# Optimization experiments

Hardware: AMD Instinct MI355X
Metric: run time of the kernel (lower is better)

## Reference

```python
import jax, jax.numpy as jnp
import numpy as np

B, CIN, H, W = 8, 256, 128, 128
DIM, K, NCLS = 32, 2048, 20
M, T = 0.999, 0.4
N_SEL = B * H * W // 2  # sal masks have exactly half foreground


def _l2norm(x, axis):
    n = jnp.sqrt(jnp.sum(x * x, axis=axis, keepdims=True))
    return x / jnp.maximum(n, 1e-12)


def _balanced_bce(logits, labels):
    # BalancedCrossEntropyLoss (astmt-style), size_average=True
    labels = (labels >= 0.5).astype(logits.dtype)
    n_pos = jnp.sum(labels)
    n_neg = labels.size - n_pos
    gz = (logits >= 0).astype(logits.dtype)
    # stable log-sigmoid formulation
    loss_val = logits * (labels - gz) - jnp.log1p(jnp.exp(logits - 2.0 * logits * gz))
    loss_pos = jnp.sum(-labels * loss_val)
    loss_neg = jnp.sum(-(1.0 - labels) * loss_val)
    tot = n_pos + n_neg
    return (n_neg / tot * loss_pos + n_pos / tot * loss_neg) / labels.size


def setup_inputs() -> dict:
    key = jax.random.key(0)
    ks = jax.random.split(key, 8)
    im_q = jax.random.normal(ks[0], (B, CIN, H, W), dtype=jnp.float32)
    im_k = jax.random.normal(ks[1], (B, CIN, H, W), dtype=jnp.float32)
    # checkerboard saliency: exactly half the pixels are foreground
    sal = (jnp.arange(B * H * W, dtype=jnp.int32) % 2).reshape(B, H, W)
    W_q = jax.random.normal(ks[2], (DIM, CIN), dtype=jnp.float32) * 0.05
    W_bg = jax.random.normal(ks[3], (1, CIN), dtype=jnp.float32) * 0.05
    W_k = jax.random.normal(ks[4], (DIM, CIN), dtype=jnp.float32) * 0.05
    W_cls = jax.random.normal(ks[5], (NCLS, DIM), dtype=jnp.float32) * 0.05
    q0 = jax.random.normal(ks[6], (DIM, K), dtype=jnp.float32)
    obj_queue = _l2norm(q0, 0)
    return {"im_q": im_q, "sal_q": sal, "im_k": im_k, "sal_k": sal,
            "W_q": W_q, "W_bg": W_bg, "W_k": W_k, "W_cls": W_cls,
            "obj_queue": obj_queue}


def reference(im_q, sal_q, im_k, sal_k, W_q, W_bg, W_k, W_cls, obj_queue):
    # --- query encoder (1x1-conv feature head + bg head) ---
    q = jnp.einsum('oc,bchw->bohw', W_q, im_q)          # [B, DIM, H, W]
    q = _l2norm(q, 1)
    q_bg = jnp.einsum('oc,bchw->bohw', W_bg, im_q)[:, 0]  # [B, H, W]
    sal_loss = _balanced_bce(q_bg, sal_q.astype(q.dtype))

    # --- classifier (1x1 conv) ---
    cluster = jnp.einsum('oc,bchw->bhwo', W_cls, q).reshape(-1, NCLS)

    # --- pixel -> image-index labeling via saliency mask ---
    offset = jnp.arange(0, 2 * B, 2, dtype=sal_q.dtype)
    lab = ((sal_q + offset[:, None, None]) * sal_q).reshape(-1)
    mask_indexes = jnp.nonzero(lab, size=N_SEL, fill_value=0)[0]
    sal_sel = lab[mask_indexes] // 2                     # [N_SEL] image index per fg pixel

    # --- momentum key encoder + object prototypes (no grad) ---
    W_k_m = M * W_k + (1.0 - M) * W_q
    k = jnp.einsum('oc,bchw->bohw', W_k_m, im_k)
    k = _l2norm(k, 1).reshape(B, DIM, H * W)
    salk = sal_k.reshape(B, H * W).astype(k.dtype)
    protos = _l2norm(jnp.einsum('bdn,bn->bd', k, salk), 1)  # [B, DIM]

    # --- gather foreground pixels ---
    q_flat = q.transpose(0, 2, 3, 1).reshape(-1, DIM)
    q_sel = q_flat[mask_indexes]                          # [N_SEL, DIM]
    cl_sel = cluster[mask_indexes]
    # opt == 2: keep only per-pixel max cluster logit, pseudo labels are zeros
    cl_sel = jnp.max(cl_sel, axis=1, keepdims=True)       # [N_SEL, 1]
    pseudo_labels = jnp.zeros((N_SEL,), dtype=jnp.int32)

    # --- contrastive logits: drop own prototype column per row ---
    batch_logits = q_sel @ protos.T                       # [N_SEL, B]
    cols = jnp.arange(B - 1)
    take = cols[None, :] + (cols[None, :] >= sal_sel[:, None]).astype(cols.dtype)
    batch_logits = jnp.take_along_axis(batch_logits, take, axis=1)  # [N_SEL, B-1]

    bank_logits = q_sel @ obj_queue                       # [N_SEL, K]
    logits = jnp.concatenate([cl_sel, batch_logits, bank_logits], axis=1) / T

    # --- dequeue-and-enqueue (ptr = 0) ---
    new_queue = jax.lax.dynamic_update_slice(obj_queue, protos.T, (0, 0))
    return logits, pseudo_labels, sal_loss, new_queue
```

## Files before the change

kernel.cpp:

```cpp
#include <hip/hip_runtime.h>

typedef __attribute__((ext_vector_type(8))) short short8;
typedef __attribute__((ext_vector_type(4))) float f32x4;
typedef __attribute__((ext_vector_type(2))) float f32x2;

constexpr int CIN  = 256;
constexpr int HWp  = 16384;
constexpr int NSEL = 65536;
constexpr int NCOLS = 2056;

constexpr size_t OUT_PL   = (size_t)NSEL * NCOLS;
constexpr size_t OUT_LOSS = OUT_PL + NSEL;
constexpr size_t OUT_NQ   = OUT_LOSS + 1;

constexpr size_t WS_TILECNT  = 0;
constexpr size_t WS_TILEBASE = 2048;
constexpr size_t WS_NPOS     = 4096;
constexpr size_t WS_LPLN     = 4104;
constexpr size_t WS_WQT      = 8192;
constexpr size_t WS_WKMT     = 40960;
constexpr size_t WS_PSUM     = 73728;
constexpr size_t WS_PROTO    = 74752;
constexpr size_t WS_QT       = 131072;
constexpr size_t WS_CLSEL    = 262144;
constexpr size_t WS_SALSEL   = 524288;
constexpr size_t WS_QSEL     = 1048576;

static __device__ __forceinline__ unsigned short f2bf(float f) {
  const unsigned x = __float_as_uint(f);
  return (unsigned short)((x + 0x7fffu + ((x >> 16) & 1u)) >> 16);
}
static __device__ __forceinline__ float bf2f(unsigned short u) {
  return __uint_as_float(((unsigned)u) << 16);
}

__global__ __launch_bounds__(256) void kP1(const int* __restrict__ salq, int* __restrict__ tileCnt,
                                           const float* __restrict__ Wq, const float* __restrict__ Wk,
                                           float* __restrict__ wqt, float* __restrict__ wkmt,
                                           float* __restrict__ psum, float* __restrict__ lpln) {
  const int g = blockIdx.x, t = threadIdx.x;
  __shared__ int red[256];
  const int base = g << 9;
  red[t] = ((salq[base + 2 * t] != 0) ? 1 : 0) + ((salq[base + 2 * t + 1] != 0) ? 1 : 0);
  __syncthreads();
  for (int s = 128; s > 0; s >>= 1) { if (t < s) red[t] += red[t + s]; __syncthreads(); }
  if (t == 0) tileCnt[g] = red[0];
  if (g < 32) {
    const int idx = (g << 8) + t;
    const int o = idx & 31, c = idx >> 5;
    const float wq = Wq[o * 256 + c];
    wqt[idx] = wq;
    wkmt[idx] = 0.999f * Wk[o * 256 + c] + 0.001f * wq;
  }
  if (g == 32) { psum[t] = 0.f; if (t < 2) lpln[t] = 0.f; }
}

__global__ __launch_bounds__(256) void kP2(const int* __restrict__ tileCnt, int* __restrict__ tileBase,
                                           int* __restrict__ nposp) {
  const int t = threadIdx.x;
  __shared__ int sc[256];
  const int c0 = tileCnt[t];
  sc[t] = c0;
  __syncthreads();
  for (int off = 1; off < 256; off <<= 1) {
    int v = (t >= off) ? sc[t - off] : 0;
    __syncthreads();
    sc[t] += v;
    __syncthreads();
  }
  tileBase[t] = sc[t] - c0;
  if (t == 255) *nposp = sc[255];
}

__global__ __launch_bounds__(256) void kAB(
    const float* __restrict__ imq, const float* __restrict__ imk,
    const int* __restrict__ salq, const int* __restrict__ salk,
    const float* __restrict__ wqt, const float* __restrict__ wkmt,
    const float* __restrict__ wbg, const float* __restrict__ wcls,
    const int* __restrict__ tileBase,
    ushort* __restrict__ qsel, float* __restrict__ clsel, int* __restrict__ salsel,
    float* __restrict__ lpln, float* __restrict__ psum) {
  const int g = ((blockIdx.x & 7) << 6) + (blockIdx.x >> 3);
  const int t = threadIdx.x;
  const bool isA = (g < 256);
  const int tile = isA ? g : (g - 256);
  const int base = tile << 9;
  const int b = base >> 14;
  const int n = (base & (HWp - 1)) + (t << 1);
  const float* __restrict__ ip = (isA ? imq : imk) + (size_t)b * (CIN * HWp) + n;
  const float* __restrict__ wt0 = isA ? wqt : wkmt;

  float a0[32], a1[32];
#pragma unroll
  for (int o = 0; o < 32; ++o) { a0[o] = 0.f; a1[o] = 0.f; }
  float bg0 = 0.f, bg1 = 0.f;

#pragma unroll 8
  for (int c = 0; c < 256; ++c) {
    const f32x2 v = __builtin_nontemporal_load(
        reinterpret_cast<const f32x2*>(ip + (size_t)c * HWp));
    const float* wt = wt0 + (c << 5);
    const float wb = wbg[c];
#pragma unroll
    for (int o = 0; o < 32; ++o) {
      a0[o] = fmaf(wt[o], v.x, a0[o]);
      a1[o] = fmaf(wt[o], v.y, a1[o]);
    }
    bg0 = fmaf(wb, v.x, bg0);
    bg1 = fmaf(wb, v.y, bg1);
  }

  const int lane = t & 63, wv = t >> 6;
  const int flat0 = base + (t << 1);

  if (isA) {
    const int s0 = (salq[flat0] != 0) ? 1 : 0;
    const int s1 = (salq[flat0 + 1] != 0) ? 1 : 0;
    const unsigned spair = (unsigned)(s0 + s1);
    unsigned incl = spair;
#pragma unroll
    for (int off = 1; off < 64; off <<= 1) {
      unsigned u = __shfl_up(incl, off);
      if (lane >= off) incl += u;
    }
    __shared__ int wtot[4];
    if (lane == 63) wtot[wv] = (int)incl;
    __syncthreads();
    int wbase = 0;
    for (int i = 0; i < wv; ++i) wbase += wtot[i];
    const int excl = tileBase[tile] + wbase + (int)(incl - spair);

#pragma unroll
    for (int i = 0; i < 2; ++i) {
      const int si = i ? s1 : s0;
      const int rank = i ? (excl + s0) : excl;
      if (si && rank < NSEL) {
        float ss = 0.f;
#pragma unroll
        for (int o = 0; o < 32; ++o) { const float a = i ? a1[o] : a0[o]; ss = fmaf(a, a, ss); }
        const float inv = 1.f / fmaxf(sqrtf(ss), 1e-12f);
        float qn[32];
#pragma unroll
        for (int o = 0; o < 32; ++o) qn[o] = (i ? a1[o] : a0[o]) * inv;
        float m = -3.402823466e38f;
#pragma unroll
        for (int j = 0; j < 20; ++j) {
          float d = 0.f;
#pragma unroll
          for (int o = 0; o < 32; ++o) d = fmaf(wcls[(j << 5) + o], qn[o], d);
          m = fmaxf(m, d);
        }
        clsel[rank] = m;
        salsel[rank] = b;
        ushort* qp = qsel + ((size_t)rank << 5);
#pragma unroll
        for (int v4 = 0; v4 < 4; ++v4) {
          short8 v8;
#pragma unroll
          for (int j = 0; j < 8; ++j) v8[j] = (short)f2bf(qn[(v4 << 3) + j]);
          *reinterpret_cast<short8*>(qp + (v4 << 3)) = v8;
        }
      }
    }
    const float gz0 = (bg0 >= 0.f) ? 1.f : 0.f;
    const float gz1 = (bg1 >= 0.f) ? 1.f : 0.f;
    const float lv0 = bg0 * ((float)s0 - gz0) - log1pf(expf(bg0 - 2.f * bg0 * gz0));
    const float lv1 = bg1 * ((float)s1 - gz1) - log1pf(expf(bg1 - 2.f * bg1 * gz1));
    float lp = -(s0 ? lv0 : 0.f) - (s1 ? lv1 : 0.f);
    float ln = -(s0 ? 0.f : lv0) - (s1 ? 0.f : lv1);
#pragma unroll
    for (int off = 32; off > 0; off >>= 1) { lp += __shfl_down(lp, off); ln += __shfl_down(ln, off); }
    __shared__ float slp[4], sln[4];
    if (lane == 0) { slp[wv] = lp; sln[wv] = ln; }
    __syncthreads();
    if (t == 0) {
      atomicAdd(&lpln[0], slp[0] + slp[1] + slp[2] + slp[3]);
      atomicAdd(&lpln[1], sln[0] + sln[1] + sln[2] + sln[3]);
    }
  } else {
    const int s0 = (salk[flat0] != 0) ? 1 : 0;
    const int s1 = (salk[flat0 + 1] != 0) ? 1 : 0;
    float ss0 = 0.f, ss1 = 0.f;
#pragma unroll
    for (int o = 0; o < 32; ++o) { ss0 = fmaf(a0[o], a0[o], ss0); ss1 = fmaf(a1[o], a1[o], ss1); }
    const float inv0 = s0 ? (1.f / fmaxf(sqrtf(ss0), 1e-12f)) : 0.f;
    const float inv1 = s1 ? (1.f / fmaxf(sqrtf(ss1), 1e-12f)) : 0.f;
    float p[32];
#pragma unroll
    for (int o = 0; o < 32; ++o) p[o] = a0[o] * inv0 + a1[o] * inv1;
#pragma unroll
    for (int o = 0; o < 32; ++o) {
#pragma unroll
      for (int off = 32; off > 0; off >>= 1) p[o] += __shfl_down(p[o], off);
    }
    __shared__ float sp[4][32];
    if (lane == 0) {
#pragma unroll
      for (int o = 0; o < 32; ++o) sp[wv][o] = p[o];
    }
    __syncthreads();
    if (t < 32) atomicAdd(&psum[(b << 5) + t], sp[0][t] + sp[1][t] + sp[2][t] + sp[3][t]);
  }
}

__global__ __launch_bounds__(256) void kC(const float* __restrict__ objq, const float* __restrict__ psum,
                                          const float* __restrict__ lpln, const int* __restrict__ nposp,
                                          float* __restrict__ proto, ushort* __restrict__ qt,
                                          float* __restrict__ nq, float* __restrict__ outLoss) {
  const int g = blockIdx.x, t = threadIdx.x;
  if (g == 256) {
    __shared__ float sq[256];
    __shared__ float sinv[8];
    const float v = psum[t];
    sq[t] = v * v;
    __syncthreads();
    if (t < 8) {
      float s = 0.f;
      for (int o = 0; o < 32; ++o) s += sq[(t << 5) + o];
      sinv[t] = 1.f / fmaxf(sqrtf(s), 1e-12f);
    }
    __syncthreads();
    const float pv = v * sinv[t >> 5];
    proto[t] = pv;
    const int p = t >> 5, o = t & 31;
    nq[(size_t)o * 2048 + p] = pv;
    if (t == 0) {
      const float np = (float)(*nposp);
      outLoss[0] = ((131072.f - np) / 131072.f * lpln[0] + np / 131072.f * lpln[1]) / 131072.f;
    }
  } else {
    const int idx = (g << 8) + t;
    const int o = idx >> 11, j = idx & 2047;
    const float v = objq[idx];
    qt[(j << 5) + o] = f2bf(v);
    if (j >= 8) nq[idx] = v;
  }
}

__global__ __launch_bounds__(256) void kDE(const ushort* __restrict__ qsel, const ushort* __restrict__ qt,
                                           const float* __restrict__ proto, const float* __restrict__ clsel,
                                           const int* __restrict__ salsel,
                                           float* __restrict__ out, int* __restrict__ pl) {
  __shared__ float buf[16][524];
  __shared__ float dd[16][9];
  const int t = threadIdx.x;
  const int g = ((blockIdx.x & 7) << 9) + (blockIdx.x >> 3);
  const int wv = t >> 6, lane = t & 63;
  const int r0 = g << 4;
  if (t < 16) pl[r0 + t] = 0;

  const int rlo = lane & 15, kh = lane >> 4;
  const f32x4 zero = {0.f, 0.f, 0.f, 0.f};

  const short8 bfrag = *reinterpret_cast<const short8*>(
      qsel + (size_t)(r0 + rlo) * 32 + kh * 8);
  const ushort* qa = qt + rlo * 32 + kh * 8;
  float* obase = out + (size_t)r0 * NCOLS;

  if (t < 128) {
    const int ri = t >> 3, pp = t & 7;
    const short8* qp = reinterpret_cast<const short8*>(qsel + ((size_t)(r0 + ri) << 5));
    float s = 0.f;
#pragma unroll
    for (int i = 0; i < 4; ++i) {
      const short8 v8 = qp[i];
#pragma unroll
      for (int j = 0; j < 8; ++j)
        s = fmaf(proto[(pp << 5) + (i << 3) + j], bf2f((unsigned short)v8[j]), s);
    }
    dd[ri][pp] = s;
  }
  __syncthreads();

  if (t < 16) {
    const int b = salsel[r0 + t];
    buf[t][0] = clsel[r0 + t] * 2.5f;
#pragma unroll
    for (int c = 0; c < 7; ++c) {
      const int pi = c + ((c >= b) ? 1 : 0);
      buf[t][1 + c] = dd[t][pi] * 2.5f;
    }
  }
#pragma unroll
  for (int ct2 = 0; ct2 < 8; ++ct2) {
    const int lt = (wv << 3) + ct2;
    const short8 afrag = *reinterpret_cast<const short8*>(qa + (size_t)lt * 512);
    f32x4 r = __builtin_amdgcn_mfma_f32_16x16x32_bf16(afrag, bfrag, zero, 0, 0, 0);
    r *= 2.5f;
    *reinterpret_cast<f32x4*>(&buf[rlo][8 + (lt << 4) + (kh << 2)]) = r;
  }
  __syncthreads();
#pragma unroll
  for (int i = 0; i < 9; ++i) {
    const int w4 = (i << 8) + t;
    if (w4 < 2080) {
      const int row = w4 / 130;
      const int c4 = w4 - row * 130;
      const f32x4 v = *reinterpret_cast<const f32x4*>(&buf[row][c4 << 2]);
      __builtin_nontemporal_store(v, reinterpret_cast<f32x4*>(obase + (size_t)row * NCOLS + (c4 << 2)));
    }
  }
  __syncthreads();

  for (int p = 1; p < 4; ++p) {
#pragma unroll
    for (int ct2 = 0; ct2 < 8; ++ct2) {
      const int lt = (wv << 3) + ct2;
      const short8 afrag = *reinterpret_cast<const short8*>(qa + (size_t)((p << 5) + lt) * 512);
      f32x4 r = __builtin_amdgcn_mfma_f32_16x16x32_bf16(afrag, bfrag, zero, 0, 0, 0);
      r *= 2.5f;
      *reinterpret_cast<f32x4*>(&buf[rlo][(lt << 4) + (kh << 2)]) = r;
    }
    __syncthreads();
    const int cbase = 8 + (p << 9);
#pragma unroll
    for (int i = 0; i < 8; ++i) {
      const int w4 = (i << 8) + t;
      const int row = w4 >> 7;
      const int c4 = w4 & 127;
      const f32x4 v = *reinterpret_cast<const f32x4*>(&buf[row][c4 << 2]);
      __builtin_nontemporal_store(v, reinterpret_cast<f32x4*>(obase + (size_t)row * NCOLS + cbase + (c4 << 2)));
    }
    __syncthreads();
  }
}

extern "C" void kernel_launch(void* const* d_in, const int* in_sizes, int n_in,
                              void* d_out, int out_size, void* d_ws, size_t ws_size,
                              hipStream_t stream) {
  const float* imq  = (const float*)d_in[0];
  const int*   salq = (const int*)d_in[1];
  const float* imk  = (const float*)d_in[2];
  const int*   salk = (const int*)d_in[3];
  const float* Wq   = (const float*)d_in[4];
  const float* Wbg  = (const float*)d_in[5];
  const float* Wk   = (const float*)d_in[6];
  const float* Wcls = (const float*)d_in[7];
  const float* objq = (const float*)d_in[8];
  float* out = (float*)d_out;
  char* ws = (char*)d_ws;

  int*    tileCnt  = (int*)(ws + WS_TILECNT);
  int*    tileBase = (int*)(ws + WS_TILEBASE);
  int*    nposp    = (int*)(ws + WS_NPOS);
  float*  lpln     = (float*)(ws + WS_LPLN);
  float*  wqt      = (float*)(ws + WS_WQT);
  float*  wkmt     = (float*)(ws + WS_WKMT);
  float*  psum     = (float*)(ws + WS_PSUM);
  float*  proto    = (float*)(ws + WS_PROTO);
  ushort* qt       = (ushort*)(ws + WS_QT);
  float*  clsel    = (float*)(ws + WS_CLSEL);
  int*    salsel   = (int*)(ws + WS_SALSEL);
  ushort* qsel     = (ushort*)(ws + WS_QSEL);

  hipLaunchKernelGGL(kP1, dim3(256), dim3(256), 0, stream, salq, tileCnt, Wq, Wk, wqt, wkmt, psum, lpln);
  hipLaunchKernelGGL(kP2, dim3(1), dim3(256), 0, stream, tileCnt, tileBase, nposp);
  hipLaunchKernelGGL(kAB, dim3(512), dim3(256), 0, stream, imq, imk, salq, salk, wqt, wkmt,
                     Wbg, Wcls, tileBase, qsel, clsel, salsel, lpln, psum);
  hipLaunchKernelGGL(kC, dim3(257), dim3(256), 0, stream, objq, psum, lpln, nposp, proto, qt,
                     out + OUT_NQ, out + OUT_LOSS);
  hipLaunchKernelGGL(kDE, dim3(4096), dim3(256), 0, stream, qsel, qt, proto, clsel, salsel,
                     out, (int*)(out + OUT_PL));
}
```

Baseline: 203.4 us.

## Prefetch next queue tile fragments and drop the barrier in the batch-logit step

The kernel now preloads the eight MFMA A-fragments for each 512-column queue chunk into registers. It issues the loads for the next chunk before the barrier and store phase, so global-load latency overlaps with the LDS readback and the output writes. The per-row batch-logit dot products are computed entirely by 16 threads with register selection, which removes the shared dd array and one __syncthreads. In exchange, register pressure rises and those 16 threads do eight times more serial work.

```diff
diff --git a/kernel.cpp b/kernel.cpp
--- a/kernel.cpp
+++ b/kernel.cpp
@@ -242,7 +242,6 @@
                                            const int* __restrict__ salsel,
                                            float* __restrict__ out, int* __restrict__ pl) {
   __shared__ float buf[16][524];
-  __shared__ float dd[16][9];
   const int t = threadIdx.x;
   const int g = ((blockIdx.x & 7) << 9) + (blockIdx.x >> 3);
   const int wv = t >> 6, lane = t & 63;
@@ -257,38 +256,51 @@
   const ushort* qa = qt + rlo * 32 + kh * 8;
   float* obase = out + (size_t)r0 * NCOLS;
 
-  if (t < 128) {
-    const int ri = t >> 3, pp = t & 7;
-    const short8* qp = reinterpret_cast<const short8*>(qsel + ((size_t)(r0 + ri) << 5));
-    float s = 0.f;
+  if (t < 16) {
+    const short8* qp = reinterpret_cast<const short8*>(qsel + ((size_t)(r0 + t) << 5));
+    float q[32];
 #pragma unroll
     for (int i = 0; i < 4; ++i) {
       const short8 v8 = qp[i];
 #pragma unroll
       for (int j = 0; j < 8; ++j)
-        s = fmaf(proto[(pp << 5) + (i << 3) + j], bf2f((unsigned short)v8[j]), s);
-    }
-    dd[ri][pp] = s;
-  }
-  __syncthreads();
-
-  if (t < 16) {
+        q[(i << 3) + j] = bf2f((unsigned short)v8[j]);
+    }
+    float d[8];
+#pragma unroll
+    for (int p = 0; p < 8; ++p) {
+      float s = 0.f;
+#pragma unroll
+      for (int o = 0; o < 32; ++o) s = fmaf(proto[(p << 5) + o], q[o], s);
+      d[p] = s;
+    }
     const int b = salsel[r0 + t];
     buf[t][0] = clsel[r0 + t] * 2.5f;
 #pragma unroll
     for (int c = 0; c < 7; ++c) {
       const int pi = c + ((c >= b) ? 1 : 0);
-      buf[t][1 + c] = dd[t][pi] * 2.5f;
-    }
-  }
-#pragma unroll
-  for (int ct2 = 0; ct2 < 8; ++ct2) {
-    const int lt = (wv << 3) + ct2;
-    const short8 afrag = *reinterpret_cast<const short8*>(qa + (size_t)lt * 512);
-    f32x4 r = __builtin_amdgcn_mfma_f32_16x16x32_bf16(afrag, bfrag, zero, 0, 0, 0);
+      float v = 0.f;
+#pragma unroll
+      for (int p = 0; p < 8; ++p) v = (p == pi) ? d[p] : v;
+      buf[t][1 + c] = v * 2.5f;
+    }
+  }
+
+  short8 af[8];
+#pragma unroll
+  for (int i = 0; i < 8; ++i)
+    af[i] = *reinterpret_cast<const short8*>(qa + (size_t)((wv << 3) + i) * 512);
+
+#pragma unroll
+  for (int i = 0; i < 8; ++i) {
+    const int lt = (wv << 3) + i;
+    f32x4 r = __builtin_amdgcn_mfma_f32_16x16x32_bf16(af[i], bfrag, zero, 0, 0, 0);
     r *= 2.5f;
     *reinterpret_cast<f32x4*>(&buf[rlo][8 + (lt << 4) + (kh << 2)]) = r;
   }
+#pragma unroll
+  for (int i = 0; i < 8; ++i)
+    af[i] = *reinterpret_cast<const short8*>(qa + (size_t)(32 + (wv << 3) + i) * 512);
   __syncthreads();
 #pragma unroll
   for (int i = 0; i < 9; ++i) {
@@ -304,12 +316,16 @@
 
   for (int p = 1; p < 4; ++p) {
 #pragma unroll
-    for (int ct2 = 0; ct2 < 8; ++ct2) {
-      const int lt = (wv << 3) + ct2;
-      const short8 afrag = *reinterpret_cast<const short8*>(qa + (size_t)((p << 5) + lt) * 512);
-      f32x4 r = __builtin_amdgcn_mfma_f32_16x16x32_bf16(afrag, bfrag, zero, 0, 0, 0);
+    for (int i = 0; i < 8; ++i) {
+      const int lt = (wv << 3) + i;
+      f32x4 r = __builtin_amdgcn_mfma_f32_16x16x32_bf16(af[i], bfrag, zero, 0, 0, 0);
       r *= 2.5f;
       *reinterpret_cast<f32x4*>(&buf[rlo][(lt << 4) + (kh << 2)]) = r;
+    }
+    if (p < 3) {
+#pragma unroll
+      for (int i = 0; i < 8; ++i)
+        af[i] = *reinterpret_cast<const short8*>(qa + (size_t)(((p + 1) << 5) + (wv << 3) + i) * 512);
     }
     __syncthreads();
     const int cbase = 8 + (p << 9);
```

Result: no change. 203.6 us (+0.1%).
